# Optimization experiments

Measured on AMD Instinct MI355X. Metric: run time of the kernel, lower is better.

## Reference

```python
import jax, jax.numpy as jnp
import numpy as np

TOKENS = 32768
DIM = 2048
N_EXPERTS = 64
TOP_K = 6
ROUTE_SCALE = 1.0


def setup_inputs() -> dict:
    key = jax.random.key(0)
    k1, k2, k3 = jax.random.split(key, 3)
    x = jax.random.normal(k1, (TOKENS, DIM), dtype=jnp.float32)
    weight = jax.random.normal(k2, (N_EXPERTS, DIM), dtype=jnp.float32) * (1.0 / np.sqrt(DIM))
    bias = jax.random.normal(k3, (N_EXPERTS,), dtype=jnp.float32) * 0.01
    return {"x": x, "weight": weight, "bias": bias}


def reference(x, weight, bias):
    # scores = F.linear(x, weight): [T, E]
    logits = jnp.einsum('td,ed->te', x, weight)
    # softmax in float32 (score_func == 'softmax')
    original_scores = jax.nn.softmax(logits.astype(jnp.float32), axis=-1)
    # bias only affects expert selection, not the returned weights
    biased = original_scores + bias
    _, indices = jax.lax.top_k(biased, TOP_K)  # [T, top_k]
    weights = jnp.take_along_axis(original_scores, indices, axis=-1)
    weights = weights * ROUTE_SCALE
    return weights.astype(x.dtype), indices
```

## Files before the change

kernel.cpp:

```cpp
#include <hip/hip_runtime.h>
#include <hip/hip_bf16.h>
#include <math.h>

#define TOKENS 32768
#define DIM    2048
#define NEXP   64
#define TOPK   6

#define BM   64
#define BK   64
#define NIT  (DIM / BK)
#define ST   72
#define PLANE (BM * ST)

typedef float f32x4 __attribute__((ext_vector_type(4)));
typedef short sh8  __attribute__((ext_vector_type(8)));

__device__ __forceinline__ ushort f2bf(float f) {
    union { __hip_bfloat16 b; ushort u; } c;
    c.b = __float2bfloat16(f);
    return c.u;
}
__device__ __forceinline__ float bf2f(ushort u) {
    union { ushort u; __hip_bfloat16 b; } c;
    c.u = u;
    return __bfloat162float(c.b);
}

__global__ __launch_bounds__(256, 2)
void gate_kernel(const float* __restrict__ x,
                 const float* __restrict__ w,
                 const float* __restrict__ bias,
                 float* __restrict__ out)
{
    __shared__ __align__(16) short smem[6 * PLANE];

    const int tid  = threadIdx.x;
    const int wave = tid >> 6;
    const int lane = tid & 63;
    const int quad = lane >> 4;
    const int l15  = lane & 15;
    const int tok0 = blockIdx.x * BM;

    const int sr = tid >> 2;
    const int sq = tid & 3;

    const float* xg = x + (long)(tok0 + sr) * DIM + sq * 16;
    const float* wg = w + (long)sr * DIM + sq * 16;

    f32x4 acc[4];
#pragma unroll
    for (int nt = 0; nt < 4; ++nt) acc[nt] = (f32x4){0.f, 0.f, 0.f, 0.f};

    float4 xf[4], wf[4];

    auto stage = [&]() {
        const int base = sr * ST + sq * 16;
#pragma unroll
        for (int g = 0; g < 2; ++g) {
            sh8 xh, xm, xl, wh, wm, wl;
#pragma unroll
            for (int i = 0; i < 8; ++i) {
                {
                    float f = ((const float*)&xf[g * 2])[i];
                    ushort h = f2bf(f);  float r1 = f - bf2f(h);
                    ushort m = f2bf(r1); float r2 = r1 - bf2f(m);
                    ushort l = f2bf(r2);
                    xh[i] = (short)h; xm[i] = (short)m; xl[i] = (short)l;
                }
                {
                    float f = ((const float*)&wf[g * 2])[i];
                    ushort h = f2bf(f);  float r1 = f - bf2f(h);
                    ushort m = f2bf(r1); float r2 = r1 - bf2f(m);
                    ushort l = f2bf(r2);
                    wh[i] = (short)h; wm[i] = (short)m; wl[i] = (short)l;
                }
            }
            *(sh8*)&smem[0 * PLANE + base + g * 8] = xh;
            *(sh8*)&smem[1 * PLANE + base + g * 8] = xm;
            *(sh8*)&smem[2 * PLANE + base + g * 8] = xl;
            *(sh8*)&smem[3 * PLANE + base + g * 8] = wh;
            *(sh8*)&smem[4 * PLANE + base + g * 8] = wm;
            *(sh8*)&smem[5 * PLANE + base + g * 8] = wl;
        }
    };

#pragma unroll
    for (int j = 0; j < 4; ++j) {
        xf[j] = *(const float4*)(xg + j * 4);
        wf[j] = *(const float4*)(wg + j * 4);
    }

    for (int it = 0; it < NIT; ++it) {
        stage();
        __syncthreads();

        if (it + 1 < NIT) {
            const int k0 = (it + 1) * BK;
#pragma unroll
            for (int j = 0; j < 4; ++j) {
                xf[j] = *(const float4*)(xg + k0 + j * 4);
                wf[j] = *(const float4*)(wg + k0 + j * 4);
            }
        }

        const int arow = (wave * 16 + l15) * ST;
#pragma unroll
        for (int ks = 0; ks < 2; ++ks) {
            const int kof = ks * 32 + quad * 8;
            sh8 ah = *(const sh8*)&smem[0 * PLANE + arow + kof];
            sh8 am = *(const sh8*)&smem[1 * PLANE + arow + kof];
            sh8 al = *(const sh8*)&smem[2 * PLANE + arow + kof];
#pragma unroll
            for (int nt = 0; nt < 4; ++nt) {
                const int brow = (nt * 16 + l15) * ST;
                sh8 bh = *(const sh8*)&smem[3 * PLANE + brow + kof];
                sh8 bm = *(const sh8*)&smem[4 * PLANE + brow + kof];
                sh8 bl = *(const sh8*)&smem[5 * PLANE + brow + kof];
                acc[nt] = __builtin_amdgcn_mfma_f32_16x16x32_bf16(ah, bh, acc[nt], 0, 0, 0);
                acc[nt] = __builtin_amdgcn_mfma_f32_16x16x32_bf16(am, bh, acc[nt], 0, 0, 0);
                acc[nt] = __builtin_amdgcn_mfma_f32_16x16x32_bf16(ah, bm, acc[nt], 0, 0, 0);
                acc[nt] = __builtin_amdgcn_mfma_f32_16x16x32_bf16(al, bh, acc[nt], 0, 0, 0);
                acc[nt] = __builtin_amdgcn_mfma_f32_16x16x32_bf16(am, bm, acc[nt], 0, 0, 0);
                acc[nt] = __builtin_amdgcn_mfma_f32_16x16x32_bf16(ah, bl, acc[nt], 0, 0, 0);
            }
        }
        __syncthreads();
    }

    float* red = (float*)smem;
#pragma unroll
    for (int nt = 0; nt < 4; ++nt)
#pragma unroll
        for (int j = 0; j < 4; ++j) {
            const int row = wave * 16 + quad * 4 + j;
            const int col = nt * 16 + l15;
            red[row * 69 + col] = acc[nt][j];
        }
    __syncthreads();

    if (tid < BM) {
        const int m = tid;
        float lg[NEXP];
#pragma unroll
        for (int e = 0; e < NEXP; ++e) lg[e] = red[m * 69 + e];

        float mx = lg[0];
#pragma unroll
        for (int e = 1; e < NEXP; ++e) mx = fmaxf(mx, lg[e]);

        float sc4[NEXP];
        float sum = 0.f;
#pragma unroll
        for (int e = 0; e < NEXP; ++e) { sc4[e] = __expf(lg[e] - mx); sum += sc4[e]; }
        const float inv = 1.0f / sum;

        float bz[NEXP];
#pragma unroll
        for (int e = 0; e < NEXP; ++e) {
            sc4[e] *= inv;
            bz[e]  = sc4[e] + bias[e];
        }

        const int tok = tok0 + m;
        float* wout = out + (long)tok * TOPK;
        float* iout = out + (long)TOKENS * TOPK + (long)tok * TOPK;

        int win[TOPK];
#pragma unroll
        for (int p = 0; p < TOPK; ++p) {
            float bmax = -INFINITY;
            int   best = 0;
            float bsc  = 0.f;
#pragma unroll
            for (int e = 0; e < NEXP; ++e) {
                bool skip = false;
#pragma unroll
                for (int pp = 0; pp < p; ++pp) skip = skip || (e == win[pp]);
                float v = skip ? -INFINITY : bz[e];
                if (v > bmax) { bmax = v; best = e; bsc = sc4[e]; }
            }
            win[p]  = best;
            wout[p] = bsc;
            iout[p] = (float)best;
        }
    }
}

extern "C" void kernel_launch(void* const* d_in, const int* in_sizes, int n_in,
                              void* d_out, int out_size, void* d_ws, size_t ws_size,
                              hipStream_t stream) {
    const float* x = (const float*)d_in[0];
    const float* w = (const float*)d_in[1];
    const float* b = (const float*)d_in[2];
    float* out = (float*)d_out;

    dim3 grid(TOKENS / BM);
    dim3 block(256);
    gate_kernel<<<grid, block, 0, stream>>>(x, w, b, out);
}
```

Measured before the change: 387.7 us.

## Presplit weights once, stream them via global_load_lds, keep x fragments in registers

A small pre-kernel splits the weight matrix into bf16 hi/mid/lo planes, stored in workspace in a swizzled layout. The gate kernel then copies those planes into double-buffered LDS with direct global-to-LDS loads. Each block no longer re-splits the weights, and x is split straight into MFMA register fragments instead of passing through LDS. The top-k epilogue is spread across all 256 threads with 4 lanes per token, using shuffle reductions in place of one thread per token. The extra launch and workspace traffic are small, but double-buffered LDS may limit occupancy.

After: 382.5 us. No clear change (-1.4%).

```diff
diff --git a/kernel.cpp b/kernel.cpp
--- a/kernel.cpp
+++ b/kernel.cpp
@@ -10,8 +10,9 @@
 #define BM   64
 #define BK   64
 #define NIT  (DIM / BK)
-#define ST   72
-#define PLANE (BM * ST)
+#define PL_SH   (NEXP * BK)
+#define CH_SH   (3 * PL_SH)
+#define CH_B    (CH_SH * 2)
 
 typedef float f32x4 __attribute__((ext_vector_type(4)));
 typedef short sh8  __attribute__((ext_vector_type(8)));
@@ -27,13 +28,44 @@
     return __bfloat162float(c.b);
 }
 
+#define GLDS(gp, lp) __builtin_amdgcn_global_load_lds( \
+    (const __attribute__((address_space(1))) void*)(gp), \
+    (__attribute__((address_space(3))) void*)(lp), 16, 0, 0)
+
+__global__ void wsplit_kernel(const float* __restrict__ w, short* __restrict__ ws)
+{
+    const int idx = blockIdx.x * 256 + threadIdx.x;
+    const int g  = idx & 7;
+    const int e  = (idx >> 3) & 63;
+    const int it = idx >> 9;
+    const int c  = g ^ (e & 7);
+
+    const float* src = w + (long)e * DIM + it * BK + c * 8;
+    float4 f0 = *(const float4*)(src);
+    float4 f1 = *(const float4*)(src + 4);
+
+    sh8 h, m, l;
+#pragma unroll
+    for (int i = 0; i < 8; ++i) {
+        float f = (i < 4) ? ((const float*)&f0)[i] : ((const float*)&f1)[i - 4];
+        ushort hh = f2bf(f);  float r1 = f - bf2f(hh);
+        ushort mm = f2bf(r1); float r2 = r1 - bf2f(mm);
+        ushort ll = f2bf(r2);
+        h[i] = (short)hh; m[i] = (short)mm; l[i] = (short)ll;
+    }
+    short* dst = ws + (long)it * CH_SH + e * BK + g * 8;
+    *(sh8*)(dst)              = h;
+    *(sh8*)(dst + PL_SH)      = m;
+    *(sh8*)(dst + 2 * PL_SH)  = l;
+}
+
 __global__ __launch_bounds__(256, 2)
 void gate_kernel(const float* __restrict__ x,
-                 const float* __restrict__ w,
+                 const short* __restrict__ ws,
                  const float* __restrict__ bias,
                  float* __restrict__ out)
 {
-    __shared__ __align__(16) short smem[6 * PLANE];
+    __shared__ __align__(16) short smem[2 * CH_SH];
 
     const int tid  = threadIdx.x;
     const int wave = tid >> 6;
@@ -42,89 +74,86 @@
     const int l15  = lane & 15;
     const int tok0 = blockIdx.x * BM;
 
-    const int sr = tid >> 2;
-    const int sq = tid & 3;
-
-    const float* xg = x + (long)(tok0 + sr) * DIM + sq * 16;
-    const float* wg = w + (long)sr * DIM + sq * 16;
+    const float* xg = x + (long)(tok0 + wave * 16 + l15) * DIM + quad * 8;
+
+    const int h8  = l15 & 7;
+    const int vb0 = l15 * 128 + (((0 * 4 + quad) ^ h8) << 4);
+    const int vb1 = l15 * 128 + (((1 * 4 + quad) ^ h8) << 4);
+    const char* sb = (const char*)smem;
 
     f32x4 acc[4];
 #pragma unroll
     for (int nt = 0; nt < 4; ++nt) acc[nt] = (f32x4){0.f, 0.f, 0.f, 0.f};
 
-    float4 xf[4], wf[4];
-
-    auto stage = [&]() {
-        const int base = sr * ST + sq * 16;
-#pragma unroll
-        for (int g = 0; g < 2; ++g) {
-            sh8 xh, xm, xl, wh, wm, wl;
+    auto stage = [&](int it, int bp) {
+        const short* s = ws + (long)it * CH_SH + tid * 8;
+        short* d = smem + bp * CH_SH + tid * 8;
+#pragma unroll
+        for (int j = 0; j < 6; ++j) GLDS(s + j * 2048, d + j * 2048);
+    };
+
+    float4 fA[4], fB[4];
+    auto loadA = [&](float4* f, int it) {
+        const float* p = xg + it * BK;
+        f[0] = *(const float4*)(p);
+        f[1] = *(const float4*)(p + 4);
+        f[2] = *(const float4*)(p + 32);
+        f[3] = *(const float4*)(p + 36);
+    };
+
+    sh8 fr[2][3];
+    auto convert = [&](const float4* f) {
+#pragma unroll
+        for (int ks = 0; ks < 2; ++ks) {
+            sh8 h, m, l;
 #pragma unroll
             for (int i = 0; i < 8; ++i) {
-                {
-                    float f = ((const float*)&xf[g * 2])[i];
-                    ushort h = f2bf(f);  float r1 = f - bf2f(h);
-                    ushort m = f2bf(r1); float r2 = r1 - bf2f(m);
-                    ushort l = f2bf(r2);
-                    xh[i] = (short)h; xm[i] = (short)m; xl[i] = (short)l;
-                }
-                {
-                    float f = ((const float*)&wf[g * 2])[i];
-                    ushort h = f2bf(f);  float r1 = f - bf2f(h);
-                    ushort m = f2bf(r1); float r2 = r1 - bf2f(m);
-                    ushort l = f2bf(r2);
-                    wh[i] = (short)h; wm[i] = (short)m; wl[i] = (short)l;
-                }
-            }
-            *(sh8*)&smem[0 * PLANE + base + g * 8] = xh;
-            *(sh8*)&smem[1 * PLANE + base + g * 8] = xm;
-            *(sh8*)&smem[2 * PLANE + base + g * 8] = xl;
-            *(sh8*)&smem[3 * PLANE + base + g * 8] = wh;
-            *(sh8*)&smem[4 * PLANE + base + g * 8] = wm;
-            *(sh8*)&smem[5 * PLANE + base + g * 8] = wl;
-        }
-    };
-
-#pragma unroll
-    for (int j = 0; j < 4; ++j) {
-        xf[j] = *(const float4*)(xg + j * 4);
-        wf[j] = *(const float4*)(wg + j * 4);
-    }
-
-    for (int it = 0; it < NIT; ++it) {
-        stage();
+                float v = ((const float*)&f[ks * 2])[i];
+                ushort hh = f2bf(v);  float r1 = v - bf2f(hh);
+                ushort mm = f2bf(r1); float r2 = r1 - bf2f(mm);
+                h[i] = (short)hh; m[i] = (short)mm; l[i] = (short)f2bf(r2);
+            }
+            fr[ks][0] = h; fr[ks][1] = m; fr[ks][2] = l;
+        }
+    };
+
+    auto compute = [&](int bufbyte) {
+#pragma unroll
+        for (int ks = 0; ks < 2; ++ks) {
+            const int va = (ks ? vb1 : vb0) + bufbyte;
+#pragma unroll
+            for (int nt = 0; nt < 4; ++nt) {
+                const int ro = va + nt * 2048;
+                sh8 bh = *(const sh8*)(sb + ro);
+                sh8 bm = *(const sh8*)(sb + ro + 8192);
+                sh8 bl = *(const sh8*)(sb + ro + 16384);
+                acc[nt] = __builtin_amdgcn_mfma_f32_16x16x32_bf16(fr[ks][0], bh, acc[nt], 0, 0, 0);
+                acc[nt] = __builtin_amdgcn_mfma_f32_16x16x32_bf16(fr[ks][1], bh, acc[nt], 0, 0, 0);
+                acc[nt] = __builtin_amdgcn_mfma_f32_16x16x32_bf16(fr[ks][0], bm, acc[nt], 0, 0, 0);
+                acc[nt] = __builtin_amdgcn_mfma_f32_16x16x32_bf16(fr[ks][2], bh, acc[nt], 0, 0, 0);
+                acc[nt] = __builtin_amdgcn_mfma_f32_16x16x32_bf16(fr[ks][1], bm, acc[nt], 0, 0, 0);
+                acc[nt] = __builtin_amdgcn_mfma_f32_16x16x32_bf16(fr[ks][0], bl, acc[nt], 0, 0, 0);
+            }
+        }
+    };
+
+    stage(0, 0);
+    loadA(fA, 0);
+    loadA(fB, 1);
+    __syncthreads();
+
+#pragma unroll 1
+    for (int it = 0; it < NIT; it += 2) {
+        stage(it + 1, 1);
+        convert(fA);
+        if (it + 2 < NIT) loadA(fA, it + 2);
+        compute(0);
         __syncthreads();
 
-        if (it + 1 < NIT) {
-            const int k0 = (it + 1) * BK;
-#pragma unroll
-            for (int j = 0; j < 4; ++j) {
-                xf[j] = *(const float4*)(xg + k0 + j * 4);
-                wf[j] = *(const float4*)(wg + k0 + j * 4);
-            }
-        }
-
-        const int arow = (wave * 16 + l15) * ST;
-#pragma unroll
-        for (int ks = 0; ks < 2; ++ks) {
-            const int kof = ks * 32 + quad * 8;
-            sh8 ah = *(const sh8*)&smem[0 * PLANE + arow + kof];
-            sh8 am = *(const sh8*)&smem[1 * PLANE + arow + kof];
-            sh8 al = *(const sh8*)&smem[2 * PLANE + arow + kof];
-#pragma unroll
-            for (int nt = 0; nt < 4; ++nt) {
-                const int brow = (nt * 16 + l15) * ST;
-                sh8 bh = *(const sh8*)&smem[3 * PLANE + brow + kof];
-                sh8 bm = *(const sh8*)&smem[4 * PLANE + brow + kof];
-                sh8 bl = *(const sh8*)&smem[5 * PLANE + brow + kof];
-                acc[nt] = __builtin_amdgcn_mfma_f32_16x16x32_bf16(ah, bh, acc[nt], 0, 0, 0);
-                acc[nt] = __builtin_amdgcn_mfma_f32_16x16x32_bf16(am, bh, acc[nt], 0, 0, 0);
-                acc[nt] = __builtin_amdgcn_mfma_f32_16x16x32_bf16(ah, bm, acc[nt], 0, 0, 0);
-                acc[nt] = __builtin_amdgcn_mfma_f32_16x16x32_bf16(al, bh, acc[nt], 0, 0, 0);
-                acc[nt] = __builtin_amdgcn_mfma_f32_16x16x32_bf16(am, bm, acc[nt], 0, 0, 0);
-                acc[nt] = __builtin_amdgcn_mfma_f32_16x16x32_bf16(ah, bl, acc[nt], 0, 0, 0);
-            }
-        }
+        if (it + 2 < NIT) stage(it + 2, 0);
+        convert(fB);
+        if (it + 3 < NIT) loadA(fB, it + 3);
+        compute(CH_B);
         __syncthreads();
     }
 
@@ -139,50 +168,57 @@
         }
     __syncthreads();
 
-    if (tid < BM) {
-        const int m = tid;
-        float lg[NEXP];
-#pragma unroll
-        for (int e = 0; e < NEXP; ++e) lg[e] = red[m * 69 + e];
+    {
+        const int t = lane >> 2;
+        const int s = lane & 3;
+        const int row = wave * 16 + t;
+
+        float lg[16];
+#pragma unroll
+        for (int i = 0; i < 16; ++i) lg[i] = red[row * 69 + s * 16 + i];
 
         float mx = lg[0];
 #pragma unroll
-        for (int e = 1; e < NEXP; ++e) mx = fmaxf(mx, lg[e]);
-
-        float sc4[NEXP];
+        for (int i = 1; i < 16; ++i) mx = fmaxf(mx, lg[i]);
+        mx = fmaxf(mx, __shfl_xor(mx, 1));
+        mx = fmaxf(mx, __shfl_xor(mx, 2));
+
         float sum = 0.f;
 #pragma unroll
-        for (int e = 0; e < NEXP; ++e) { sc4[e] = __expf(lg[e] - mx); sum += sc4[e]; }
+        for (int i = 0; i < 16; ++i) { lg[i] = __expf(lg[i] - mx); sum += lg[i]; }
+        sum += __shfl_xor(sum, 1);
+        sum += __shfl_xor(sum, 2);
         const float inv = 1.0f / sum;
 
-        float bz[NEXP];
-#pragma unroll
-        for (int e = 0; e < NEXP; ++e) {
-            sc4[e] *= inv;
-            bz[e]  = sc4[e] + bias[e];
-        }
-
-        const int tok = tok0 + m;
+        float sc[16], bz[16];
+#pragma unroll
+        for (int i = 0; i < 16; ++i) {
+            sc[i] = lg[i] * inv;
+            bz[i] = sc[i] + bias[s * 16 + i];
+        }
+
+        const int tok = tok0 + wave * 16 + t;
         float* wout = out + (long)tok * TOPK;
         float* iout = out + (long)TOKENS * TOPK + (long)tok * TOPK;
 
-        int win[TOPK];
+        unsigned used = 0;
 #pragma unroll
         for (int p = 0; p < TOPK; ++p) {
-            float bmax = -INFINITY;
-            int   best = 0;
-            float bsc  = 0.f;
-#pragma unroll
-            for (int e = 0; e < NEXP; ++e) {
-                bool skip = false;
-#pragma unroll
-                for (int pp = 0; pp < p; ++pp) skip = skip || (e == win[pp]);
-                float v = skip ? -INFINITY : bz[e];
-                if (v > bmax) { bmax = v; best = e; bsc = sc4[e]; }
-            }
-            win[p]  = best;
-            wout[p] = bsc;
-            iout[p] = (float)best;
+            float bv = -INFINITY; int bi = 1 << 20; float bw = 0.f;
+#pragma unroll
+            for (int i = 0; i < 16; ++i) {
+                float v = ((used >> i) & 1u) ? -INFINITY : bz[i];
+                if (v > bv) { bv = v; bi = s * 16 + i; bw = sc[i]; }
+            }
+#pragma unroll
+            for (int d = 1; d < 4; d <<= 1) {
+                float ov = __shfl_xor(bv, d);
+                int   oi = __shfl_xor(bi, d);
+                float ow = __shfl_xor(bw, d);
+                if (ov > bv || (ov == bv && oi < bi)) { bv = ov; bi = oi; bw = ow; }
+            }
+            if ((bi >> 4) == s) used |= 1u << (bi & 15);
+            if (s == 0) { wout[p] = bw; iout[p] = (float)bi; }
         }
     }
 }
@@ -194,8 +230,8 @@
     const float* w = (const float*)d_in[1];
     const float* b = (const float*)d_in[2];
     float* out = (float*)d_out;
-
-    dim3 grid(TOKENS / BM);
-    dim3 block(256);
-    gate_kernel<<<grid, block, 0, stream>>>(x, w, b, out);
-}
+    short* ws = (short*)d_ws;
+
+    wsplit_kernel<<<dim3(64), dim3(256), 0, stream>>>(w, ws);
+    gate_kernel<<<dim3(TOKENS / BM), dim3(256), 0, stream>>>(x, ws, b, out);
+}
```
